# Kernel tuning notes

Measured on AMD Instinct MI355X. Metric: run time of the kernel, lower is better.

Reference implementation:

```python
import jax, jax.numpy as jnp
import numpy as np

B, T, D = 1, 2048, 2048
H, G, HD = 16, 4, 128          # num_heads, num_kv_groups, head_dim
GS = H // G                    # group_size
EPS = 1e-6


def rmsnorm(x, w):
    return x * jax.lax.rsqrt(jnp.mean(x * x, axis=-1, keepdims=True) + EPS) * w


def apply_rope(x, cos, sin, offset=0):
    # x: [B, heads, T, HD]; cos/sin: [max_seq, HD]
    t = x.shape[2]
    c = cos[offset:offset + t][None, None]  # [1,1,T,HD]
    s = sin[offset:offset + t][None, None]
    x1, x2 = x[..., : HD // 2], x[..., HD // 2:]
    rot = jnp.concatenate([-x2, x1], axis=-1)
    return x * c + rot * s


def setup_inputs() -> dict:
    key = jax.random.key(0)
    ks = jax.random.split(key, 8)
    x = jax.random.normal(ks[0], (B, T, D), dtype=jnp.float32)
    # causal mask: True = masked out
    mask = jnp.triu(jnp.ones((T, T), dtype=bool), k=1)[None, None]
    # RoPE tables (theta=10000), duplicated-halves layout
    inv_freq = 1.0 / (10000.0 ** (jnp.arange(0, HD, 2, dtype=jnp.float32) / HD))
    angles = jnp.arange(T, dtype=jnp.float32)[:, None] * inv_freq[None, :]  # [T, HD/2]
    angles = jnp.concatenate([angles, angles], axis=-1)                     # [T, HD]
    cos, sin = jnp.cos(angles), jnp.sin(angles)
    sc = 0.02
    Wq = jax.random.normal(ks[1], (H * HD, D), dtype=jnp.float32) * sc
    Wk = jax.random.normal(ks[2], (G * HD, D), dtype=jnp.float32) * sc
    Wv = jax.random.normal(ks[3], (G * HD, D), dtype=jnp.float32) * sc
    Wo = jax.random.normal(ks[4], (D, H * HD), dtype=jnp.float32) * sc
    q_norm_w = jnp.ones((H * HD,), dtype=jnp.float32)
    k_norm_w = jnp.ones((G * HD,), dtype=jnp.float32)
    return {"x": x, "mask": mask, "cos": cos, "sin": sin,
            "Wq": Wq, "Wk": Wk, "Wv": Wv, "Wo": Wo,
            "q_norm_w": q_norm_w, "k_norm_w": k_norm_w}


def reference(x, mask, cos, sin, Wq, Wk, Wv, Wo, q_norm_w, k_norm_w):
    b, t, _ = x.shape
    q = rmsnorm(x @ Wq.T, q_norm_w)   # [B,T,H*HD]
    k = rmsnorm(x @ Wk.T, k_norm_w)   # [B,T,G*HD]
    v = x @ Wv.T                      # [B,T,G*HD]
    q = q.reshape(b, t, H, HD).transpose(0, 2, 1, 3)   # [B,H,T,HD]
    k = k.reshape(b, t, G, HD).transpose(0, 2, 1, 3)   # [B,G,T,HD]
    v = v.reshape(b, t, G, HD).transpose(0, 2, 1, 3)
    q = apply_rope(q, cos, sin, offset=0)
    k = apply_rope(k, cos, sin, offset=0)
    # GQA: repeat_interleave KV heads to match query heads
    k = jnp.repeat(k, GS, axis=1)     # [B,H,T,HD]
    vr = jnp.repeat(v, GS, axis=1)
    q = q * (HD ** -0.5)
    scores = jnp.einsum('bhqd,bhkd->bhqk', q, k)        # [B,H,T,T]
    scores = jnp.where(mask, -jnp.inf, scores)
    attn = jax.nn.softmax(scores, axis=-1)
    ctx = jnp.einsum('bhqk,bhkd->bhqd', attn, vr)
    ctx = ctx.transpose(0, 2, 1, 3).reshape(b, t, H * HD)
    return ctx @ Wo.T                                   # [B,T,D]
```

## Files before the change

kernel.cpp:

```cpp
#include <hip/hip_runtime.h>

#define T_SEQ 2048
#define DMODEL 2048
#define NHEADS 16
#define NKV 4
#define HDIM 128
#define KVDIM (NKV*HDIM)
#define QKVN (DMODEL + 2*KVDIM)

typedef __bf16 bf16x8 __attribute__((ext_vector_type(8)));
typedef float f32x4 __attribute__((ext_vector_type(4)));
typedef unsigned short us8 __attribute__((ext_vector_type(8)));
typedef unsigned short ushort_t;

__device__ __forceinline__ ushort_t f2b(float f) {
    union { float f; unsigned u; } c; c.f = f;
    unsigned r = c.u + 0x7FFFu + ((c.u >> 16) & 1u);
    return (ushort_t)(r >> 16);
}
__device__ __forceinline__ ushort_t f2b_rn(float f) {
    union { __bf16 h; ushort_t u; } c; c.h = (__bf16)f; return c.u;
}
__device__ __forceinline__ float b2f(ushort_t b) {
    union { unsigned u; float f; } c; c.u = ((unsigned)b) << 16; return c.f;
}

#define GLDS(g, l) __builtin_amdgcn_global_load_lds( \
    (const __attribute__((address_space(1))) void*)(g), \
    (__attribute__((address_space(3))) void*)(l), 16, 0, 0)

__global__ __launch_bounds__(256) void cvt5_kernel(
    const float* __restrict__ s0, ushort_t* __restrict__ d0, int c0,
    const float* __restrict__ s1, ushort_t* __restrict__ d1, int c1,
    const float* __restrict__ s2, ushort_t* __restrict__ d2, int c2,
    const float* __restrict__ s3, ushort_t* __restrict__ d3, int c3,
    const float* __restrict__ s4, ushort_t* __restrict__ d4, int c4)
{
    int u = blockIdx.x * 256 + threadIdx.x;
    const float* s; ushort_t* d; int off;
    if      (u < c0) { s = s0; d = d0; off = u; }
    else if (u < c1) { s = s1; d = d1; off = u - c0; }
    else if (u < c2) { s = s2; d = d2; off = u - c1; }
    else if (u < c3) { s = s3; d = d3; off = u - c2; }
    else if (u < c4) { s = s4; d = d4; off = u - c3; }
    else return;
    const float4 v = *(const float4*)(s + off * 4);
    ushort4 o = make_ushort4(f2b(v.x), f2b(v.y), f2b(v.z), f2b(v.w));
    *(ushort4*)(d + off * 4) = o;
}

template<int MODE>
__global__ __launch_bounds__(256) void gemm_bt(
    const ushort_t* __restrict__ A, const ushort_t* __restrict__ B,
    ushort_t* __restrict__ Cb, float* __restrict__ Cf, ushort_t* __restrict__ VT,
    int M, int N, int K)
{
    __shared__ ushort_t As[128 * 64];
    __shared__ ushort_t Bs[128 * 64];
    const int tid = threadIdx.x;
    const int lane = tid & 63;
    const int wv = tid >> 6;
    const int wr = wv >> 1, wc = wv & 1;
    const int lrow = lane & 15, lhi = lane >> 4;
    const int m0 = blockIdx.y * 128, n0 = blockIdx.x * 128;

    f32x4 acc[4][4];
#pragma unroll
    for (int i = 0; i < 4; i++)
#pragma unroll
        for (int j = 0; j < 4; j++) acc[i][j] = f32x4{0.f, 0.f, 0.f, 0.f};

    const int srow = tid >> 3;
    const int scol = (tid & 7) * 8;

    for (int kt = 0; kt < K; kt += 64) {
        if (kt) __syncthreads();
#pragma unroll
        for (int r = 0; r < 4; ++r) {
            int row = srow + r * 32;
            GLDS(A + (size_t)(m0 + row) * K + kt + scol, As + row * 64 + scol);
            GLDS(B + (size_t)(n0 + row) * K + kt + scol, Bs + row * 64 + scol);
        }
        __syncthreads();
#pragma unroll
        for (int kk = 0; kk < 2; ++kk) {
            bf16x8 af[4], bfr[4];
#pragma unroll
            for (int i = 0; i < 4; i++)
                af[i] = *(const bf16x8*)(As + (wr * 64 + i * 16 + lrow) * 64 + kk * 32 + lhi * 8);
#pragma unroll
            for (int j = 0; j < 4; j++)
                bfr[j] = *(const bf16x8*)(Bs + (wc * 64 + j * 16 + lrow) * 64 + kk * 32 + lhi * 8);
#pragma unroll
            for (int i = 0; i < 4; i++)
#pragma unroll
                for (int j = 0; j < 4; j++)
                    acc[i][j] = __builtin_amdgcn_mfma_f32_16x16x32_bf16(af[i], bfr[j], acc[i][j], 0, 0, 0);
        }
    }
    if (MODE == 2 && n0 >= DMODEL + KVDIM) {
#pragma unroll
        for (int i = 0; i < 4; i++)
#pragma unroll
            for (int j = 0; j < 4; j++) {
                int col = n0 + wc * 64 + j * 16 + lrow - (DMODEL + KVDIM);
                int row0 = m0 + wr * 64 + i * 16 + lhi * 4;
                ushort4 pk = make_ushort4(f2b(acc[i][j][0]), f2b(acc[i][j][1]),
                                          f2b(acc[i][j][2]), f2b(acc[i][j][3]));
                *(ushort4*)(VT + (size_t)col * T_SEQ + row0) = pk;
            }
    } else {
#pragma unroll
        for (int i = 0; i < 4; i++)
#pragma unroll
            for (int j = 0; j < 4; j++)
#pragma unroll
                for (int e = 0; e < 4; e++) {
                    int row = m0 + wr * 64 + i * 16 + lhi * 4 + e;
                    int col = n0 + wc * 64 + j * 16 + lrow;
                    if (MODE == 1) Cf[(size_t)row * N + col] = acc[i][j][e];
                    else           Cb[(size_t)row * N + col] = f2b(acc[i][j][e]);
                }
    }
}

template<int DROW>
__device__ __forceinline__ void norm_rope_body(
    const ushort_t* __restrict__ src, int sld, int scol,
    const float* __restrict__ w,
    const float* __restrict__ cosT, const float* __restrict__ sinT,
    ushort_t* __restrict__ dst, int dld, float oscale,
    float* rowbuf, float* red)
{
    constexpr int PER = DROW / 256;
    const int tid = threadIdx.x;
    const int t = blockIdx.x;
    const ushort_t* rp = src + (size_t)t * sld + scol;
    const int e0 = tid * PER;

    float vals[PER];
    if constexpr (PER == 8) {
        us8 u = *(const us8*)(rp + e0);
#pragma unroll
        for (int p = 0; p < PER; p++) vals[p] = b2f(u[p]);
    } else {
        ushort2 u = *(const ushort2*)(rp + e0);
        vals[0] = b2f(u.x); vals[1] = b2f(u.y);
    }
    float ss = 0.f;
#pragma unroll
    for (int p = 0; p < PER; p++) { ss += vals[p] * vals[p]; rowbuf[e0 + p] = vals[p]; }
#pragma unroll
    for (int o = 32; o; o >>= 1) ss += __shfl_down(ss, o);
    if ((tid & 63) == 0) red[tid >> 6] = ss;
    __syncthreads();
    float rn = rsqrtf((red[0] + red[1] + red[2] + red[3]) / (float)DROW + 1e-6f);
#pragma unroll
    for (int p = 0; p < PER; p++) {
        int e = e0 + p, r = e & 127;
        float c = cosT[t * HDIM + r], s = sinT[t * HDIM + r];
        int pe = (r < 64) ? e + 64 : e - 64;
        float self = rowbuf[e] * rn * w[e];
        float part = rowbuf[pe] * rn * w[pe];
        float o = (r < 64) ? (self * c - part * s) : (self * c + part * s);
        dst[(size_t)t * dld + e] = f2b(o * oscale);
    }
}

__global__ __launch_bounds__(256) void norm_rope_qk(
    const ushort_t* __restrict__ qkv,
    const float* __restrict__ qw, const float* __restrict__ kw,
    const float* __restrict__ cosT, const float* __restrict__ sinT,
    ushort_t* __restrict__ qb, ushort_t* __restrict__ kb)
{
    __shared__ float rowbuf[DMODEL];
    __shared__ float red[4];
    if (blockIdx.y == 0)
        norm_rope_body<DMODEL>(qkv, QKVN, 0, qw, cosT, sinT, qb, DMODEL,
                               0.08838834764831843f, rowbuf, red);
    else
        norm_rope_body<KVDIM>(qkv, QKVN, DMODEL, kw, cosT, sinT, kb, KVDIM,
                              1.0f, rowbuf, red);
}

__global__ __launch_bounds__(128, 2) void fattn(
    const ushort_t* __restrict__ Q,
    const ushort_t* __restrict__ Kb,
    const ushort_t* __restrict__ VT,
    ushort_t* __restrict__ ctx)
{
    __shared__ ushort_t Ks[2][32 * 128];
    __shared__ ushort_t Vt[2][128 * 32];
    __shared__ ushort_t Pw[2][16 * 32];
    const int tid = threadIdx.x, lane = tid & 63, wv = tid >> 6;
    const int lrow = lane & 15, lhi = lane >> 4;
    const int h = blockIdx.x;
    const int qt = 63 - (int)blockIdx.y;
    const int g = h >> 2;
    const int q0 = qt * 32;
    const int sw = (lrow >> 1) & 3;
    const int kswz = lrow & 7;

    const int srK = tid >> 4, scK = tid & 15;
    const int srV = tid >> 2, scV = tid & 3;

    bf16x8 qf[4];
    {
        int qr = q0 + wv * 16 + lrow;
#pragma unroll
        for (int ks = 0; ks < 4; ks++)
            qf[ks] = *(const bf16x8*)(Q + (size_t)qr * DMODEL + h * HDIM + ks * 32 + lhi * 8);
    }
    f32x4 of[8];
#pragma unroll
    for (int f = 0; f < 8; f++) of[f] = f32x4{0.f, 0.f, 0.f, 0.f};
    float m_ = -1e30f, l_ = 0.f;
    const int myq = q0 + wv * 16 + lrow;

    auto stage = [&](int kt, int b) {
        const int k0 = kt * 32;
#pragma unroll
        for (int r = 0; r < 4; r++) {
            int row = r * 8 + srK;
            GLDS(Kb + (size_t)(k0 + row) * KVDIM + g * HDIM + ((scK ^ (row & 7)) << 3),
                 Ks[b] + row * 128 + (scK << 3));
        }
#pragma unroll
        for (int r = 0; r < 4; r++) {
            int row = r * 32 + srV;
            GLDS(VT + (size_t)(g * HDIM + row) * T_SEQ + k0 + ((scV ^ ((row >> 1) & 3)) << 3),
                 Vt[b] + row * 32 + (scV << 3));
        }
    };

    stage(0, 0);
    __syncthreads();
    int buf = 0;

    for (int kt = 0; kt <= qt; ++kt) {
        if (kt < qt) stage(kt + 1, buf ^ 1);
        const ushort_t* KsB = Ks[buf];
        const ushort_t* VtB = Vt[buf];
        const int k0 = kt * 32;

        f32x4 sf[2];
        sf[0] = f32x4{0.f, 0.f, 0.f, 0.f};
        sf[1] = f32x4{0.f, 0.f, 0.f, 0.f};
#pragma unroll
        for (int ks = 0; ks < 4; ks++) {
#pragma unroll
            for (int nf = 0; nf < 2; nf++) {
                bf16x8 kf = *(const bf16x8*)(KsB + (nf * 16 + lrow) * 128 +
                                             (((ks * 4 + lhi) ^ kswz) << 3));
                sf[nf] = __builtin_amdgcn_mfma_f32_16x16x32_bf16(kf, qf[ks], sf[nf], 0, 0, 0);
            }
        }
#pragma unroll
        for (int nf = 0; nf < 2; nf++)
#pragma unroll
            for (int j = 0; j < 4; j++)
                if (k0 + nf * 16 + lhi * 4 + j > myq) sf[nf][j] = -1e30f;
        float mx = fmaxf(fmaxf(fmaxf(sf[0][0], sf[0][1]), fmaxf(sf[0][2], sf[0][3])),
                         fmaxf(fmaxf(sf[1][0], sf[1][1]), fmaxf(sf[1][2], sf[1][3])));
        mx = fmaxf(mx, __shfl_xor(mx, 16));
        mx = fmaxf(mx, __shfl_xor(mx, 32));
        if (!__all(mx - m_ <= 8.0f)) {
            float mn = fmaxf(m_, mx);
            float sc = __expf(m_ - mn);
            m_ = mn;
            l_ *= sc;
            float scb[4];
#pragma unroll
            for (int j = 0; j < 4; j++) scb[j] = __shfl(sc, lhi * 4 + j);
#pragma unroll
            for (int f = 0; f < 8; f++)
#pragma unroll
                for (int j = 0; j < 4; j++) of[f][j] *= scb[j];
        }
        float pf[2][4];
#pragma unroll
        for (int nf = 0; nf < 2; nf++)
#pragma unroll
            for (int j = 0; j < 4; j++) {
                pf[nf][j] = __expf(sf[nf][j] - m_);
                l_ += pf[nf][j];
            }
#pragma unroll
        for (int nf = 0; nf < 2; nf++) {
            ushort4 pk = make_ushort4(f2b_rn(pf[nf][0]), f2b_rn(pf[nf][1]),
                                      f2b_rn(pf[nf][2]), f2b_rn(pf[nf][3]));
            int u = 2 * nf + (lhi >> 1);
            *(ushort4*)(Pw[wv] + lrow * 32 + ((u ^ sw) << 3) + ((lhi & 1) << 2)) = pk;
        }
        bf16x8 pa = *(const bf16x8*)(Pw[wv] + lrow * 32 + ((lhi ^ sw) << 3));
#pragma unroll
        for (int f = 0; f < 8; f++) {
            bf16x8 vf = *(const bf16x8*)(VtB + (f * 16 + lrow) * 32 + ((lhi ^ sw) << 3));
            of[f] = __builtin_amdgcn_mfma_f32_16x16x32_bf16(pa, vf, of[f], 0, 0, 0);
        }
        __syncthreads();
        buf ^= 1;
    }
    l_ += __shfl_xor(l_, 16);
    l_ += __shfl_xor(l_, 32);
    float lb[4];
#pragma unroll
    for (int j = 0; j < 4; j++) lb[j] = __shfl(l_, lhi * 4 + j);
#pragma unroll
    for (int f = 0; f < 8; f++)
#pragma unroll
        for (int j = 0; j < 4; j++) {
            int qrow = q0 + wv * 16 + lhi * 4 + j;
            ctx[(size_t)qrow * DMODEL + h * HDIM + f * 16 + lrow] = f2b_rn(of[f][j] / lb[j]);
        }
}

extern "C" void kernel_launch(void* const* d_in, const int* in_sizes, int n_in,
                              void* d_out, int out_size, void* d_ws, size_t ws_size,
                              hipStream_t stream)
{
    const float* x    = (const float*)d_in[0];
    const float* cosT = (const float*)d_in[2];
    const float* sinT = (const float*)d_in[3];
    const float* Wq   = (const float*)d_in[4];
    const float* Wk   = (const float*)d_in[5];
    const float* Wv   = (const float*)d_in[6];
    const float* Wo   = (const float*)d_in[7];
    const float* qw   = (const float*)d_in[8];
    const float* kw   = (const float*)d_in[9];
    float* out = (float*)d_out;

    char* ws = (char*)d_ws;
    size_t off = 0;
    auto alloc = [&](size_t bytes) -> char* {
        char* p = ws + off; off += (bytes + 255) & ~(size_t)255; return p;
    };
    ushort_t* xb    = (ushort_t*)alloc((size_t)T_SEQ * DMODEL * 2);
    ushort_t* wqkvb = (ushort_t*)alloc((size_t)QKVN * DMODEL * 2);
    ushort_t* wob   = (ushort_t*)alloc((size_t)DMODEL * DMODEL * 2);
    ushort_t* qkvb  = (ushort_t*)alloc((size_t)T_SEQ * QKVN * 2);
    ushort_t* qb    = (ushort_t*)alloc((size_t)T_SEQ * DMODEL * 2);
    ushort_t* kb    = (ushort_t*)alloc((size_t)T_SEQ * KVDIM * 2);
    ushort_t* ctxb  = (ushort_t*)alloc((size_t)T_SEQ * DMODEL * 2);
    ushort_t* vtb   = (ushort_t*)alloc((size_t)KVDIM * T_SEQ * 2);

    const int n_x  = T_SEQ * DMODEL / 4;
    const int n_wq = DMODEL * DMODEL / 4;
    const int n_wk = KVDIM * DMODEL / 4;
    const int n_wv = KVDIM * DMODEL / 4;
    const int n_wo = DMODEL * DMODEL / 4;
    const int c0 = n_x, c1 = c0 + n_wq, c2 = c1 + n_wk, c3 = c2 + n_wv, c4 = c3 + n_wo;
    cvt5_kernel<<<dim3((c4 + 255) / 256), dim3(256), 0, stream>>>(
        x,  xb, c0,
        Wq, wqkvb, c1,
        Wk, wqkvb + (size_t)DMODEL * DMODEL, c2,
        Wv, wqkvb + (size_t)(DMODEL + KVDIM) * DMODEL, c3,
        Wo, wob, c4);

    gemm_bt<2><<<dim3(QKVN / 128, T_SEQ / 128), dim3(256), 0, stream>>>(
        xb, wqkvb, qkvb, nullptr, vtb, T_SEQ, QKVN, DMODEL);

    norm_rope_qk<<<dim3(T_SEQ, 2), dim3(256), 0, stream>>>(
        qkvb, qw, kw, cosT, sinT, qb, kb);

    fattn<<<dim3(NHEADS, 64), dim3(128), 0, stream>>>(qb, kb, vtb, ctxb);

    gemm_bt<1><<<dim3(DMODEL / 128, T_SEQ / 128), dim3(256), 0, stream>>>(
        ctxb, wob, nullptr, out, nullptr, T_SEQ, DMODEL, DMODEL);
}
```

Before: 296.9 us.

## Triple-buffer K/V tiles in flash attention with explicit vmcnt waits

Switches the attention kernel's K/V shared-memory staging from double to triple buffering. Loads now run two tiles ahead, and an explicit s_waitcnt vmcnt(8) waits only for the older tile's async loads before a bare s_barrier, instead of a full __syncthreads. The goal is to hide global-load latency behind the MFMA work. In exchange, shared memory per block grows and the min-blocks-per-CU launch bound is dropped. The hand-counted vmcnt and the sched barriers also depend on the exact number of outstanding loads per stage.

```diff
diff --git a/kernel.cpp b/kernel.cpp
--- a/kernel.cpp
+++ b/kernel.cpp
@@ -183,14 +183,14 @@
                               1.0f, rowbuf, red);
 }
 
-__global__ __launch_bounds__(128, 2) void fattn(
+__global__ __launch_bounds__(128) void fattn(
     const ushort_t* __restrict__ Q,
     const ushort_t* __restrict__ Kb,
     const ushort_t* __restrict__ VT,
     ushort_t* __restrict__ ctx)
 {
-    __shared__ ushort_t Ks[2][32 * 128];
-    __shared__ ushort_t Vt[2][128 * 32];
+    __shared__ ushort_t Ks[3][32 * 128];
+    __shared__ ushort_t Vt[3][128 * 32];
     __shared__ ushort_t Pw[2][16 * 32];
     const int tid = threadIdx.x, lane = tid & 63, wv = tid >> 6;
     const int lrow = lane & 15, lhi = lane >> 4;
@@ -234,13 +234,19 @@
     };
 
     stage(0, 0);
-    __syncthreads();
-    int buf = 0;
+    if (qt >= 1) {
+        stage(1, 1);
+        asm volatile("s_waitcnt vmcnt(8)" ::: "memory");
+    } else {
+        asm volatile("s_waitcnt vmcnt(0)" ::: "memory");
+    }
+    __builtin_amdgcn_s_barrier();
+    __builtin_amdgcn_sched_barrier(0);
 
     for (int kt = 0; kt <= qt; ++kt) {
-        if (kt < qt) stage(kt + 1, buf ^ 1);
-        const ushort_t* KsB = Ks[buf];
-        const ushort_t* VtB = Vt[buf];
+        const int b = kt - (kt / 3) * 3;
+        const ushort_t* KsB = Ks[b];
+        const ushort_t* VtB = Vt[b];
         const int k0 = kt * 32;
 
         f32x4 sf[2];
@@ -298,8 +304,17 @@
             bf16x8 vf = *(const bf16x8*)(VtB + (f * 16 + lrow) * 32 + ((lhi ^ sw) << 3));
             of[f] = __builtin_amdgcn_mfma_f32_16x16x32_bf16(pa, vf, of[f], 0, 0, 0);
         }
-        __syncthreads();
-        buf ^= 1;
+
+        const int rem = qt - kt;
+        if (rem == 0) break;
+        if (rem >= 2) {
+            stage(kt + 2, (kt + 2) - ((kt + 2) / 3) * 3);
+            asm volatile("s_waitcnt vmcnt(8)" ::: "memory");
+        } else {
+            asm volatile("s_waitcnt vmcnt(0)" ::: "memory");
+        }
+        __builtin_amdgcn_s_barrier();
+        __builtin_amdgcn_sched_barrier(0);
     }
     l_ += __shfl_xor(l_, 16);
     l_ += __shfl_xor(l_, 32);
```

After: 296.2 us. Within noise of the previous version (-0.2%).
